# Performance work log

Hardware: AMD Instinct MI355X
Metric: run time of the kernel (lower is better)

Reference implementation:

```python
import jax, jax.numpy as jnp
import numpy as np

B, D = 4096, 512
BASE_TAU = 0.02
CLAMP_MAX = 1e36


def _l2norm(x, eps=1e-12):
    # torch F.normalize(p=2): x / max(||x||, eps)
    n = jnp.sqrt(jnp.sum(x * x, axis=-1, keepdims=True))
    return x / jnp.maximum(n, eps)


def setup_inputs() -> dict:
    key = jax.random.key(0)
    k1, k2, k3, k4, k5, k6 = jax.random.split(key, 6)
    return {
        "visual_feats": jax.random.normal(k1, (B, D), dtype=jnp.float32),
        "textual_feats": jax.random.normal(k2, (B, D), dtype=jnp.float32),
        "pid": jax.random.randint(k3, (B,), 0, 1024, dtype=jnp.int64 if jax.config.jax_enable_x64 else jnp.int32),
        "adaptive_margins": jax.random.uniform(k4, (B,), dtype=jnp.float32),
        "uncertainty_scores": jax.random.uniform(k5, (B,), dtype=jnp.float32),
        "sample_types": jax.random.randint(k6, (B,), 0, 3, dtype=jnp.int64 if jax.config.jax_enable_x64 else jnp.int32),
    }


def reference(visual_feats, textual_feats, pid, adaptive_margins, uncertainty_scores, sample_types):
    tau = BASE_TAU
    vn = _l2norm(visual_feats)
    tn = _l2norm(textual_feats)
    scores = tn @ vn.T  # [B, B]

    # Faithful to the original loop: every iteration i builds a [B,B] matrix
    # whose rows are all scores[i,:] and uses the FULL pid vector, then takes
    # row 0 of the per-sample loss. So the label/mask row is always pid[0]'s.
    labels0 = (pid == pid[0]).astype(scores.dtype)  # [B]
    mask0 = 1.0 - labels0                            # [B]
    n_neg0 = jnp.sum(mask0)

    margins = jax.lax.stop_gradient(adaptive_margins)  # .item() in torch -> no grad

    e = jnp.exp(scores / tau)  # [B, B]
    # i2t branch (row 0 of expanded matrix == scores[i,:], mask row = mask0)
    alpha = jax.lax.stop_gradient(e * labels0 / jnp.sum(e * labels0, axis=1, keepdims=True))  # [B,B]
    neg_sum = jnp.minimum(jnp.sum(e * mask0, axis=1), CLAMP_MAX)  # [B]
    loss_i2t = jnp.maximum(-jnp.sum(alpha * scores, axis=1) + tau * jnp.log(neg_sum) + margins, 0.0)

    # t2i branch: row 0 of expanded.T is scores[i,0] repeated B times;
    # alpha_t2i row 0 sums to 1 so -(alpha*s).sum == -scores[i,0].
    s0 = scores[:, 0]  # [B]
    t2i_sum = jnp.minimum(jnp.exp(s0 / tau) * n_neg0, CLAMP_MAX)
    loss_t2i = jnp.maximum(-s0 + tau * jnp.log(t2i_sum) + margins, 0.0)

    per_sample_losses = loss_i2t + loss_t2i  # [B]

    uncertain = sample_types == 2
    uncertainty_weights = jnp.where(
        uncertain,
        jnp.clip(1.0 - 0.5 * uncertainty_scores, 0.1, 1.0),
        jnp.ones_like(uncertainty_scores),
    )
    final_loss = jnp.sum(per_sample_losses * uncertainty_weights) / jnp.sum(uncertainty_weights)
    return final_loss, per_sample_losses, uncertainty_weights, scores
```

## Files before the change

### kernel.cpp

```cpp
#include <hip/hip_runtime.h>
#include <hip/hip_bf16.h>
#include <stdint.h>

#define NB 4096
#define ND 512
#define TAU_ 0.02f
#define INV_TAU_ 50.0f
#define CLAMP_MAXF 1e36f

typedef __attribute__((ext_vector_type(8))) short bf16x8;
typedef __attribute__((ext_vector_type(4))) float f32x4;

#define AS1(p) ((__attribute__((address_space(1))) void*)(uintptr_t)(p))
#define AS3(p) ((__attribute__((address_space(3))) void*)(uint32_t)(uintptr_t)(p))

static __device__ __forceinline__ unsigned short f2bf(float f) {
  __hip_bfloat16 h = __float2bfloat16(f);
  return *reinterpret_cast<unsigned short*>(&h);
}

__global__ __launch_bounds__(256) void k_norm(const float* __restrict__ vis,
                                              const float* __restrict__ txt,
                                              const int* __restrict__ pid,
                                              unsigned short* __restrict__ tn_b,
                                              unsigned short* __restrict__ vn_b,
                                              float* __restrict__ nneg) {
  if (blockIdx.x == 2048) {
    __shared__ float r4[4];
    int tid = threadIdx.x;
    int pid0 = pid[0];
    float c = 0.f;
    for (int j = tid; j < NB; j += 256) c += (pid[j] != pid0) ? 1.0f : 0.0f;
#pragma unroll
    for (int o = 32; o; o >>= 1) c += __shfl_xor(c, o, 64);
    if ((tid & 63) == 0) r4[tid >> 6] = c;
    __syncthreads();
    if (tid == 0) nneg[0] = r4[0] + r4[1] + r4[2] + r4[3];
    return;
  }
  int wv = threadIdx.x >> 6, ln = threadIdx.x & 63;
  int r = blockIdx.x * 4 + wv;
  const float* src;
  unsigned short* dst;
  if (r < NB) {
    src = txt + (size_t)r * ND;
    dst = tn_b + (size_t)r * ND;
  } else {
    src = vis + (size_t)(r - NB) * ND;
    dst = vn_b + (size_t)(r - NB) * ND;
  }
  float4 x0 = reinterpret_cast<const float4*>(src)[ln];
  float4 x1 = reinterpret_cast<const float4*>(src)[64 + ln];
  float ss = x0.x * x0.x + x0.y * x0.y + x0.z * x0.z + x0.w * x0.w +
             x1.x * x1.x + x1.y * x1.y + x1.z * x1.z + x1.w * x1.w;
#pragma unroll
  for (int o = 32; o; o >>= 1) ss += __shfl_xor(ss, o, 64);
  float inv = 1.0f / fmaxf(sqrtf(ss), 1e-12f);
  ushort4 p0, p1;
  p0.x = f2bf(x0.x * inv); p0.y = f2bf(x0.y * inv);
  p0.z = f2bf(x0.z * inv); p0.w = f2bf(x0.w * inv);
  p1.x = f2bf(x1.x * inv); p1.y = f2bf(x1.y * inv);
  p1.z = f2bf(x1.z * inv); p1.w = f2bf(x1.w * inv);
  reinterpret_cast<ushort4*>(dst)[ln] = p0;
  reinterpret_cast<ushort4*>(dst)[64 + ln] = p1;
}

__global__ __launch_bounds__(512, 2) void k_gemm(const unsigned short* __restrict__ A,
                                                 const unsigned short* __restrict__ Bm,
                                                 const int* __restrict__ pid,
                                                 float* __restrict__ C,
                                                 float* __restrict__ partials) {
  __shared__ unsigned short smem[2][2][256 * 64];
  int tid = threadIdx.x;
  int wv = tid >> 6, ln = tid & 63;
  int bm = blockIdx.x >> 4;
  int bn = blockIdx.x & 15;
  int wr = wv >> 2, wc = wv & 3;
  int frow = ln & 15, fkg = ln >> 4;
  f32x4 acc[8][4] = {};
  const unsigned short* Abase = A + (size_t)(bm * 256) * ND;
  const unsigned short* Bbase = Bm + (size_t)(bn * 256) * ND;

#define STAGE(buf, k0)                                                          \
  {                                                                             \
    _Pragma("unroll") for (int p = 0; p < 4; ++p) {                             \
      int s = p * 512 + tid;                                                    \
      int rr = s >> 3;                                                          \
      int slot = (s & 7) ^ (rr & 7);            \
      __builtin_amdgcn_global_load_lds(                                         \
          AS1(Abase + (size_t)rr * ND + (k0) + slot * 8),                       \
          AS3((char*)&smem[buf][0][0] + (p * 512 + wv * 64) * 16), 16, 0, 0);   \
      __builtin_amdgcn_global_load_lds(                                         \
          AS1(Bbase + (size_t)rr * ND + (k0) + slot * 8),                       \
          AS3((char*)&smem[buf][1][0] + (p * 512 + wv * 64) * 16), 16, 0, 0);   \
    }                                                                           \
  }

  STAGE(0, 0);
  __syncthreads();
  int buf = 0;
  for (int t = 0; t < 8; ++t) {
    if (t < 7) STAGE(buf ^ 1, (t + 1) * 64);
    const char* pA = (const char*)&smem[buf][0][0];
    const char* pB = (const char*)&smem[buf][1][0];
#pragma unroll
    for (int ksub = 0; ksub < 2; ++ksub) {
      bf16x8 af[8], bfr[4];
#pragma unroll
      for (int mi = 0; mi < 8; ++mi) {
        int row = wr * 128 + mi * 16 + frow;
        af[mi] = *reinterpret_cast<const bf16x8*>(
            pA + row * 128 + (((ksub * 4 + fkg) ^ (row & 7)) * 16));
      }
#pragma unroll
      for (int ni = 0; ni < 4; ++ni) {
        int row = wc * 64 + ni * 16 + frow;
        bfr[ni] = *reinterpret_cast<const bf16x8*>(
            pB + row * 128 + (((ksub * 4 + fkg) ^ (row & 7)) * 16));
      }
#pragma unroll
      for (int mi = 0; mi < 8; ++mi)
#pragma unroll
        for (int ni = 0; ni < 4; ++ni)
          acc[mi][ni] = __builtin_amdgcn_mfma_f32_16x16x32_bf16(af[mi], bfr[ni],
                                                                acc[mi][ni], 0, 0, 0);
    }
    __syncthreads();
    buf ^= 1;
  }

  int pid0 = pid[0];
  int eq[4];
#pragma unroll
  for (int ni = 0; ni < 4; ++ni)
    eq[ni] = (pid[bn * 256 + wc * 64 + ni * 16 + frow] == pid0) ? 1 : 0;

  float* pb = reinterpret_cast<float*>(&smem[0][0][0]);
  float* Cp = C + (size_t)(bm * 256 + wr * 128 + fkg * 4) * NB + bn * 256 +
              wc * 64 + frow;
#pragma unroll
  for (int mi = 0; mi < 8; ++mi) {
#pragma unroll
    for (int v = 0; v < 4; ++v) {
      float sp = 0.f, sn = 0.f, sa = 0.f;
      float* rp = Cp + (size_t)(mi * 16 + v) * NB;
#pragma unroll
      for (int ni = 0; ni < 4; ++ni) {
        float s = acc[mi][ni][v];
        rp[ni * 16] = s;
        float e = __expf(s * INV_TAU_);
        if (eq[ni]) {
          sp += e;
          sa += e * s;
        } else {
          sn += e;
        }
      }
#pragma unroll
      for (int o = 1; o < 16; o <<= 1) {
        sp += __shfl_xor(sp, o, 64);
        sn += __shfl_xor(sn, o, 64);
        sa += __shfl_xor(sa, o, 64);
      }
      if (frow == 0) {
        int row = wr * 128 + mi * 16 + fkg * 4 + v;
        pb[(wc * 256 + row) * 3 + 0] = sp;
        pb[(wc * 256 + row) * 3 + 1] = sn;
        pb[(wc * 256 + row) * 3 + 2] = sa;
      }
    }
  }
  __syncthreads();
  if (tid < 256) {
    float sp = 0.f, sn = 0.f, sa = 0.f;
#pragma unroll
    for (int w = 0; w < 4; ++w) {
      sp += pb[(w * 256 + tid) * 3 + 0];
      sn += pb[(w * 256 + tid) * 3 + 1];
      sa += pb[(w * 256 + tid) * 3 + 2];
    }
    float* pout = partials + ((size_t)(bm * 256 + tid) * 16 + bn) * 3;
    pout[0] = sp;
    pout[1] = sn;
    pout[2] = sa;
  }
}

__global__ __launch_bounds__(256) void k_row2(const float* __restrict__ partials,
                                              const float* __restrict__ scores,
                                              const float* __restrict__ margins,
                                              const float* __restrict__ unc,
                                              const int* __restrict__ stypes,
                                              const float* __restrict__ nneg,
                                              float* __restrict__ psl,
                                              float* __restrict__ uw) {
  int wv = threadIdx.x >> 6, ln = threadIdx.x & 63;
  int row = blockIdx.x * 4 + wv;
  const float* p = partials + (size_t)row * 16 * 3;
  float sp = 0.f, sn = 0.f, sa = 0.f;
  if (ln < 16) {
    sp = p[ln * 3 + 0];
    sn = p[ln * 3 + 1];
    sa = p[ln * 3 + 2];
  }
#pragma unroll
  for (int o = 1; o < 16; o <<= 1) {
    sp += __shfl_xor(sp, o, 64);
    sn += __shfl_xor(sn, o, 64);
    sa += __shfl_xor(sa, o, 64);
  }
  if (ln == 0) {
    float s0v = scores[(size_t)row * NB];
    float m = margins[row];
    float li2t = fmaxf(-(sa / sp) + TAU_ * logf(fminf(sn, CLAMP_MAXF)) + m, 0.f);
    float t2i = fminf(__expf(s0v * INV_TAU_) * nneg[0], CLAMP_MAXF);
    float lt2i = fmaxf(-s0v + TAU_ * logf(t2i) + m, 0.f);
    psl[row] = li2t + lt2i;
    float w = 1.f;
    if (stypes[row] == 2) w = fminf(fmaxf(1.f - 0.5f * unc[row], 0.1f), 1.f);
    uw[row] = w;
  }
}

__global__ __launch_bounds__(256) void k_final(const float* __restrict__ psl,
                                               const float* __restrict__ uw,
                                               float* __restrict__ out) {
  __shared__ float rn[4], rd[4];
  int tid = threadIdx.x;
  float num = 0.f, den = 0.f;
  for (int j = tid; j < NB; j += 256) {
    float w = uw[j];
    num += psl[j] * w;
    den += w;
  }
#pragma unroll
  for (int o = 32; o; o >>= 1) {
    num += __shfl_xor(num, o, 64);
    den += __shfl_xor(den, o, 64);
  }
  if ((tid & 63) == 0) {
    rn[tid >> 6] = num;
    rd[tid >> 6] = den;
  }
  __syncthreads();
  if (tid == 0) {
    num = rn[0] + rn[1] + rn[2] + rn[3];
    den = rd[0] + rd[1] + rd[2] + rd[3];
    out[0] = num / den;
  }
}

extern "C" void kernel_launch(void* const* d_in, const int* in_sizes, int n_in,
                              void* d_out, int out_size, void* d_ws, size_t ws_size,
                              hipStream_t stream) {
  const float* vis = (const float*)d_in[0];
  const float* txt = (const float*)d_in[1];
  const int* pid = (const int*)d_in[2];
  const float* margins = (const float*)d_in[3];
  const float* unc = (const float*)d_in[4];
  const int* stypes = (const int*)d_in[5];

  float* out = (float*)d_out;
  float* out_psl = out + 1;
  float* out_uw = out + 1 + NB;
  float* out_scores = out + 1 + 2 * NB;

  unsigned short* tn_b = (unsigned short*)d_ws;
  unsigned short* vn_b = tn_b + (size_t)NB * ND;
  float* nneg = (float*)(vn_b + (size_t)NB * ND);
  float* partials = nneg + 4;

  k_norm<<<2049, 256, 0, stream>>>(vis, txt, pid, tn_b, vn_b, nneg);
  k_gemm<<<256, 512, 0, stream>>>(tn_b, vn_b, pid, out_scores, partials);
  k_row2<<<NB / 4, 256, 0, stream>>>(partials, out_scores, margins, unc, stypes,
                                     nneg, out_psl, out_uw);
  k_final<<<1, 256, 0, stream>>>(out_psl, out_uw, out);
}
```

Measured before the change: 51.01 us.

## Deepen GEMM K-pipeline to 4-stage ring with BK=32, tile swizzle and setprio

Restructures the GEMM main loop from a double-buffered BK=64 scheme into a 4-buffer ring of BK=32 stages, keeping two loads in flight and synchronising with explicit vmcnt waits and a single barrier per step. It also changes the LDS swizzle to a rotation pattern suited to 64-byte rows, remaps block indices so neighbouring blocks share A/B tiles in cache, and raises wave priority around the MFMA burst. The aim is to hide global-to-LDS latency better and cut barrier overhead. The handwritten vmcnt counts are fragile and the per-step MFMA work is halved.

```diff
diff --git a/kernel.cpp b/kernel.cpp
--- a/kernel.cpp
+++ b/kernel.cpp
@@ -70,64 +70,67 @@
                                                  const int* __restrict__ pid,
                                                  float* __restrict__ C,
                                                  float* __restrict__ partials) {
-  __shared__ unsigned short smem[2][2][256 * 64];
+  __shared__ unsigned short smem[4][2][256 * 32];
   int tid = threadIdx.x;
   int wv = tid >> 6, ln = tid & 63;
-  int bm = blockIdx.x >> 4;
-  int bn = blockIdx.x & 15;
+  int tile = (blockIdx.x & 7) * 32 + (blockIdx.x >> 3);
+  int bm = tile >> 4;
+  int bn = tile & 15;
   int wr = wv >> 2, wc = wv & 3;
   int frow = ln & 15, fkg = ln >> 4;
   f32x4 acc[8][4] = {};
   const unsigned short* Abase = A + (size_t)(bm * 256) * ND;
   const unsigned short* Bbase = Bm + (size_t)(bn * 256) * ND;
 
-#define STAGE(buf, k0)                                                          \
+#define STAGE(bidx, k0)                                                         \
   {                                                                             \
-    _Pragma("unroll") for (int p = 0; p < 4; ++p) {                             \
+    _Pragma("unroll") for (int p = 0; p < 2; ++p) {                             \
       int s = p * 512 + tid;                                                    \
-      int rr = s >> 3;                                                          \
-      int slot = (s & 7) ^ (rr & 7);            \
+      int rr = s >> 2;                                                          \
+      int sg = ((s & 3) + (rr >> 1)) & 3;                                       \
       __builtin_amdgcn_global_load_lds(                                         \
-          AS1(Abase + (size_t)rr * ND + (k0) + slot * 8),                       \
-          AS3((char*)&smem[buf][0][0] + (p * 512 + wv * 64) * 16), 16, 0, 0);   \
+          AS1(Abase + (size_t)rr * ND + (k0) + sg * 8),                         \
+          AS3((char*)&smem[bidx][0][0] + (p * 512 + wv * 64) * 16), 16, 0, 0);  \
       __builtin_amdgcn_global_load_lds(                                         \
-          AS1(Bbase + (size_t)rr * ND + (k0) + slot * 8),                       \
-          AS3((char*)&smem[buf][1][0] + (p * 512 + wv * 64) * 16), 16, 0, 0);   \
+          AS1(Bbase + (size_t)rr * ND + (k0) + sg * 8),                         \
+          AS3((char*)&smem[bidx][1][0] + (p * 512 + wv * 64) * 16), 16, 0, 0);  \
     }                                                                           \
   }
 
+#define COMPUTE(bidx)                                                           \
+  {                                                                             \
+    const char* pA = (const char*)&smem[bidx][0][0];                            \
+    const char* pB = (const char*)&smem[bidx][1][0];                            \
+    bf16x8 af[8], bfr[4];                                                       \
+    _Pragma("unroll") for (int mi = 0; mi < 8; ++mi) {                          \
+      int row = wr * 128 + mi * 16 + frow;                                      \
+      af[mi] = *reinterpret_cast<const bf16x8*>(                                \
+          pA + row * 64 + (((fkg - (row >> 1)) & 3) * 16));                     \
+    }                                                                           \
+    _Pragma("unroll") for (int ni = 0; ni < 4; ++ni) {                          \
+      int row = wc * 64 + ni * 16 + frow;                                       \
+      bfr[ni] = *reinterpret_cast<const bf16x8*>(                               \
+          pB + row * 64 + (((fkg - (row >> 1)) & 3) * 16));                     \
+    }                                                                           \
+    __builtin_amdgcn_s_setprio(1);                                              \
+    _Pragma("unroll") for (int mi = 0; mi < 8; ++mi)                            \
+      _Pragma("unroll") for (int ni = 0; ni < 4; ++ni)                          \
+        acc[mi][ni] = __builtin_amdgcn_mfma_f32_16x16x32_bf16(af[mi], bfr[ni],  \
+                                                              acc[mi][ni], 0, 0, 0); \
+    __builtin_amdgcn_s_setprio(0);                                              \
+  }
+
   STAGE(0, 0);
-  __syncthreads();
-  int buf = 0;
-  for (int t = 0; t < 8; ++t) {
-    if (t < 7) STAGE(buf ^ 1, (t + 1) * 64);
-    const char* pA = (const char*)&smem[buf][0][0];
-    const char* pB = (const char*)&smem[buf][1][0];
-#pragma unroll
-    for (int ksub = 0; ksub < 2; ++ksub) {
-      bf16x8 af[8], bfr[4];
-#pragma unroll
-      for (int mi = 0; mi < 8; ++mi) {
-        int row = wr * 128 + mi * 16 + frow;
-        af[mi] = *reinterpret_cast<const bf16x8*>(
-            pA + row * 128 + (((ksub * 4 + fkg) ^ (row & 7)) * 16));
-      }
-#pragma unroll
-      for (int ni = 0; ni < 4; ++ni) {
-        int row = wc * 64 + ni * 16 + frow;
-        bfr[ni] = *reinterpret_cast<const bf16x8*>(
-            pB + row * 128 + (((ksub * 4 + fkg) ^ (row & 7)) * 16));
-      }
-#pragma unroll
-      for (int mi = 0; mi < 8; ++mi)
-#pragma unroll
-        for (int ni = 0; ni < 4; ++ni)
-          acc[mi][ni] = __builtin_amdgcn_mfma_f32_16x16x32_bf16(af[mi], bfr[ni],
-                                                                acc[mi][ni], 0, 0, 0);
-    }
-    __syncthreads();
-    buf ^= 1;
-  }
+  STAGE(1, 32);
+  for (int t = 0; t < 15; ++t) {
+    asm volatile("s_waitcnt vmcnt(4)" ::: "memory");
+    __builtin_amdgcn_s_barrier();
+    if (t < 14) STAGE((t + 2) & 3, (t + 2) * 32);
+    COMPUTE(t & 3);
+  }
+  asm volatile("s_waitcnt vmcnt(0)" ::: "memory");
+  __builtin_amdgcn_s_barrier();
+  COMPUTE(3);
 
   int pid0 = pid[0];
   int eq[4];
```

After: 52.14 us. 2.2% more time.

## Add dedicated producer wave with LDS flag handshake for GEMM K-loop loads

Applied to the files above, without the earlier changes.

Adds a ninth wavefront to the GEMM block that only issues global-to-LDS loads into the double buffer. It signals compute waves through workgroup-scope atomic flags instead of block-wide __syncthreads, so loads overlap MFMA work without a full-block barrier each K step. The change also swizzles block-to-tile mapping, writes per-wave partials straight to global memory (64 per row, reduced in k_row2) instead of through LDS, and exports column-0 scores to a small buffer. The costs are spin-wait polling, lower occupancy from the 576-thread block without the min-blocks hint, and more partial-sum traffic.

```diff
diff --git a/kernel.cpp b/kernel.cpp
--- a/kernel.cpp
+++ b/kernel.cpp
@@ -65,53 +65,70 @@
   reinterpret_cast<ushort4*>(dst)[64 + ln] = p1;
 }
 
-__global__ __launch_bounds__(512, 2) void k_gemm(const unsigned short* __restrict__ A,
-                                                 const unsigned short* __restrict__ Bm,
-                                                 const int* __restrict__ pid,
-                                                 float* __restrict__ C,
-                                                 float* __restrict__ partials) {
+__global__ __launch_bounds__(576) void k_gemm(const unsigned short* __restrict__ A,
+                                              const unsigned short* __restrict__ Bm,
+                                              const int* __restrict__ pid,
+                                              float* __restrict__ C,
+                                              float* __restrict__ partials,
+                                              float* __restrict__ s0g) {
   __shared__ unsigned short smem[2][2][256 * 64];
+  __shared__ unsigned int flg[4];
   int tid = threadIdx.x;
   int wv = tid >> 6, ln = tid & 63;
-  int bm = blockIdx.x >> 4;
-  int bn = blockIdx.x & 15;
+  int tile = (blockIdx.x & 7) * 32 + (blockIdx.x >> 3);
+  int bm = tile >> 4, bn = tile & 15;
+  const unsigned short* Abase = A + (size_t)(bm * 256) * ND;
+  const unsigned short* Bbase = Bm + (size_t)(bn * 256) * ND;
+  if (tid < 4) flg[tid] = 0;
+  __syncthreads();
+
+  if (wv == 8) {
+    int lanerow = ln >> 3;
+    int slot = (ln & 7) ^ (lanerow & 7);
+    const unsigned short* srcA = Abase + (size_t)lanerow * ND + slot * 8;
+    const unsigned short* srcB = Bbase + (size_t)lanerow * ND + slot * 8;
+    for (int j = 0; j < 8; ++j) {
+      if (j >= 2) {
+        unsigned need = (unsigned)((j >> 1) * 8);
+        while (__hip_atomic_load(&flg[2 + (j & 1)], __ATOMIC_ACQUIRE,
+                                 __HIP_MEMORY_SCOPE_WORKGROUP) < need)
+          __builtin_amdgcn_s_sleep(1);
+      }
+      int b = j & 1;
+      const unsigned short* sA = srcA + j * 64;
+      const unsigned short* sB = srcB + j * 64;
+      char* dA = (char*)&smem[b][0][0];
+      char* dB = (char*)&smem[b][1][0];
+#pragma unroll 8
+      for (int i = 0; i < 32; ++i)
+        __builtin_amdgcn_global_load_lds(AS1(sA + (size_t)i * 8 * ND),
+                                         AS3(dA + i * 1024), 16, 0, 0);
+#pragma unroll 8
+      for (int i = 0; i < 32; ++i)
+        __builtin_amdgcn_global_load_lds(AS1(sB + (size_t)i * 8 * ND),
+                                         AS3(dB + i * 1024), 16, 0, 0);
+      asm volatile("s_waitcnt vmcnt(0)" ::: "memory");
+      __builtin_amdgcn_sched_barrier(0);
+      __hip_atomic_store(&flg[b], (unsigned)(j + 1), __ATOMIC_RELEASE,
+                         __HIP_MEMORY_SCOPE_WORKGROUP);
+    }
+    return;
+  }
+
   int wr = wv >> 2, wc = wv & 3;
   int frow = ln & 15, fkg = ln >> 4;
   f32x4 acc[8][4] = {};
-  const unsigned short* Abase = A + (size_t)(bm * 256) * ND;
-  const unsigned short* Bbase = Bm + (size_t)(bn * 256) * ND;
-
-#define STAGE(buf, k0)                                                          \
-  {                                                                             \
-    _Pragma("unroll") for (int p = 0; p < 4; ++p) {                             \
-      int s = p * 512 + tid;                                                    \
-      int rr = s >> 3;                                                          \
-      int slot = (s & 7) ^ (rr & 7);            \
-      __builtin_amdgcn_global_load_lds(                                         \
-          AS1(Abase + (size_t)rr * ND + (k0) + slot * 8),                       \
-          AS3((char*)&smem[buf][0][0] + (p * 512 + wv * 64) * 16), 16, 0, 0);   \
-      __builtin_amdgcn_global_load_lds(                                         \
-          AS1(Bbase + (size_t)rr * ND + (k0) + slot * 8),                       \
-          AS3((char*)&smem[buf][1][0] + (p * 512 + wv * 64) * 16), 16, 0, 0);   \
-    }                                                                           \
-  }
-
-  STAGE(0, 0);
-  __syncthreads();
-  int buf = 0;
-  for (int t = 0; t < 8; ++t) {
-    if (t < 7) STAGE(buf ^ 1, (t + 1) * 64);
-    const char* pA = (const char*)&smem[buf][0][0];
-    const char* pB = (const char*)&smem[buf][1][0];
+
+  for (int j = 0; j < 8; ++j) {
+    while (__hip_atomic_load(&flg[j & 1], __ATOMIC_ACQUIRE,
+                             __HIP_MEMORY_SCOPE_WORKGROUP) < (unsigned)(j + 1))
+      __builtin_amdgcn_s_sleep(1);
+    __builtin_amdgcn_sched_barrier(0);
+    const char* pA = (const char*)&smem[j & 1][0][0];
+    const char* pB = (const char*)&smem[j & 1][1][0];
 #pragma unroll
     for (int ksub = 0; ksub < 2; ++ksub) {
-      bf16x8 af[8], bfr[4];
-#pragma unroll
-      for (int mi = 0; mi < 8; ++mi) {
-        int row = wr * 128 + mi * 16 + frow;
-        af[mi] = *reinterpret_cast<const bf16x8*>(
-            pA + row * 128 + (((ksub * 4 + fkg) ^ (row & 7)) * 16));
-      }
+      bf16x8 bfr[4];
 #pragma unroll
       for (int ni = 0; ni < 4; ++ni) {
         int row = wc * 64 + ni * 16 + frow;
@@ -119,14 +136,21 @@
             pB + row * 128 + (((ksub * 4 + fkg) ^ (row & 7)) * 16));
       }
 #pragma unroll
-      for (int mi = 0; mi < 8; ++mi)
+      for (int mi = 0; mi < 8; ++mi) {
+        int row = wr * 128 + mi * 16 + frow;
+        bf16x8 a_ = *reinterpret_cast<const bf16x8*>(
+            pA + row * 128 + (((ksub * 4 + fkg) ^ (row & 7)) * 16));
 #pragma unroll
         for (int ni = 0; ni < 4; ++ni)
-          acc[mi][ni] = __builtin_amdgcn_mfma_f32_16x16x32_bf16(af[mi], bfr[ni],
-                                                                acc[mi][ni], 0, 0, 0);
+          acc[mi][ni] = __builtin_amdgcn_mfma_f32_16x16x32_bf16(a_, bfr[ni],
+                                                               acc[mi][ni], 0, 0, 0);
+      }
     }
-    __syncthreads();
-    buf ^= 1;
+    asm volatile("s_waitcnt lgkmcnt(0)" ::: "memory");
+    __builtin_amdgcn_sched_barrier(0);
+    if (ln == 0)
+      __hip_atomic_fetch_add(&flg[2 + (j & 1)], 1u, __ATOMIC_RELEASE,
+                             __HIP_MEMORY_SCOPE_WORKGROUP);
   }
 
   int pid0 = pid[0];
@@ -134,8 +158,6 @@
 #pragma unroll
   for (int ni = 0; ni < 4; ++ni)
     eq[ni] = (pid[bn * 256 + wc * 64 + ni * 16 + frow] == pid0) ? 1 : 0;
-
-  float* pb = reinterpret_cast<float*>(&smem[0][0][0]);
   float* Cp = C + (size_t)(bm * 256 + wr * 128 + fkg * 4) * NB + bn * 256 +
               wc * 64 + frow;
 #pragma unroll
@@ -163,31 +185,19 @@
         sa += __shfl_xor(sa, o, 64);
       }
       if (frow == 0) {
-        int row = wr * 128 + mi * 16 + fkg * 4 + v;
-        pb[(wc * 256 + row) * 3 + 0] = sp;
-        pb[(wc * 256 + row) * 3 + 1] = sn;
-        pb[(wc * 256 + row) * 3 + 2] = sa;
+        int row = bm * 256 + wr * 128 + mi * 16 + fkg * 4 + v;
+        float* po = partials + ((size_t)row * 64 + bn * 4 + wc) * 3;
+        po[0] = sp;
+        po[1] = sn;
+        po[2] = sa;
+        if (bn == 0 && wc == 0) s0g[row] = acc[mi][0][v];
       }
     }
   }
-  __syncthreads();
-  if (tid < 256) {
-    float sp = 0.f, sn = 0.f, sa = 0.f;
-#pragma unroll
-    for (int w = 0; w < 4; ++w) {
-      sp += pb[(w * 256 + tid) * 3 + 0];
-      sn += pb[(w * 256 + tid) * 3 + 1];
-      sa += pb[(w * 256 + tid) * 3 + 2];
-    }
-    float* pout = partials + ((size_t)(bm * 256 + tid) * 16 + bn) * 3;
-    pout[0] = sp;
-    pout[1] = sn;
-    pout[2] = sa;
-  }
 }
 
 __global__ __launch_bounds__(256) void k_row2(const float* __restrict__ partials,
-                                              const float* __restrict__ scores,
+                                              const float* __restrict__ s0g,
                                               const float* __restrict__ margins,
                                               const float* __restrict__ unc,
                                               const int* __restrict__ stypes,
@@ -196,21 +206,16 @@
                                               float* __restrict__ uw) {
   int wv = threadIdx.x >> 6, ln = threadIdx.x & 63;
   int row = blockIdx.x * 4 + wv;
-  const float* p = partials + (size_t)row * 16 * 3;
-  float sp = 0.f, sn = 0.f, sa = 0.f;
-  if (ln < 16) {
-    sp = p[ln * 3 + 0];
-    sn = p[ln * 3 + 1];
-    sa = p[ln * 3 + 2];
-  }
-#pragma unroll
-  for (int o = 1; o < 16; o <<= 1) {
+  const float* p = partials + (size_t)row * 64 * 3 + ln * 3;
+  float sp = p[0], sn = p[1], sa = p[2];
+#pragma unroll
+  for (int o = 1; o < 64; o <<= 1) {
     sp += __shfl_xor(sp, o, 64);
     sn += __shfl_xor(sn, o, 64);
     sa += __shfl_xor(sa, o, 64);
   }
   if (ln == 0) {
-    float s0v = scores[(size_t)row * NB];
+    float s0v = s0g[row];
     float m = margins[row];
     float li2t = fmaxf(-(sa / sp) + TAU_ * logf(fminf(sn, CLAMP_MAXF)) + m, 0.f);
     float t2i = fminf(__expf(s0v * INV_TAU_) * nneg[0], CLAMP_MAXF);
@@ -268,11 +273,12 @@
   unsigned short* tn_b = (unsigned short*)d_ws;
   unsigned short* vn_b = tn_b + (size_t)NB * ND;
   float* nneg = (float*)(vn_b + (size_t)NB * ND);
-  float* partials = nneg + 4;
+  float* s0g = nneg + 4;
+  float* partials = s0g + NB;
 
   k_norm<<<2049, 256, 0, stream>>>(vis, txt, pid, tn_b, vn_b, nneg);
-  k_gemm<<<256, 512, 0, stream>>>(tn_b, vn_b, pid, out_scores, partials);
-  k_row2<<<NB / 4, 256, 0, stream>>>(partials, out_scores, margins, unc, stypes,
+  k_gemm<<<256, 576, 0, stream>>>(tn_b, vn_b, pid, out_scores, partials, s0g);
+  k_row2<<<NB / 4, 256, 0, stream>>>(partials, s0g, margins, unc, stypes,
                                      nneg, out_psl, out_uw);
   k_final<<<1, 256, 0, stream>>>(out_psl, out_uw, out);
 }
```

Measured after the change: 66.85 us. +31.0%, slower.

## Remap GEMM tiles across XCDs, stream scores non-temporally, drop LDS epilogue reduction

Applied to the files above, without the earlier changes.

Block indices are remapped so that consecutive tiles sharing A/B panels land on the same XCD, aiming for better L2 reuse. The score matrix is now written with nontemporal stores so it does not pollute the cache. The in-block LDS reduction and its barrier are removed: each wave writes its own partial sums straight to global memory, and the row kernel reduces 64 partials per row. Column-0 scores go to a small side buffer so the row kernel no longer does strided reads from the large output. In exchange, the partials buffer is four times larger.

```diff
diff --git a/kernel.cpp b/kernel.cpp
--- a/kernel.cpp
+++ b/kernel.cpp
@@ -69,12 +69,14 @@
                                                  const unsigned short* __restrict__ Bm,
                                                  const int* __restrict__ pid,
                                                  float* __restrict__ C,
-                                                 float* __restrict__ partials) {
+                                                 float* __restrict__ partials,
+                                                 float* __restrict__ s0g) {
   __shared__ unsigned short smem[2][2][256 * 64];
   int tid = threadIdx.x;
   int wv = tid >> 6, ln = tid & 63;
-  int bm = blockIdx.x >> 4;
-  int bn = blockIdx.x & 15;
+  int tile = (blockIdx.x & 7) * 32 + (blockIdx.x >> 3);
+  int bm = tile >> 4;
+  int bn = tile & 15;
   int wr = wv >> 2, wc = wv & 3;
   int frow = ln & 15, fkg = ln >> 4;
   f32x4 acc[8][4] = {};
@@ -134,8 +136,6 @@
 #pragma unroll
   for (int ni = 0; ni < 4; ++ni)
     eq[ni] = (pid[bn * 256 + wc * 64 + ni * 16 + frow] == pid0) ? 1 : 0;
-
-  float* pb = reinterpret_cast<float*>(&smem[0][0][0]);
   float* Cp = C + (size_t)(bm * 256 + wr * 128 + fkg * 4) * NB + bn * 256 +
               wc * 64 + frow;
 #pragma unroll
@@ -147,7 +147,7 @@
 #pragma unroll
       for (int ni = 0; ni < 4; ++ni) {
         float s = acc[mi][ni][v];
-        rp[ni * 16] = s;
+        __builtin_nontemporal_store(s, rp + ni * 16);
         float e = __expf(s * INV_TAU_);
         if (eq[ni]) {
           sp += e;
@@ -163,31 +163,19 @@
         sa += __shfl_xor(sa, o, 64);
       }
       if (frow == 0) {
-        int row = wr * 128 + mi * 16 + fkg * 4 + v;
-        pb[(wc * 256 + row) * 3 + 0] = sp;
-        pb[(wc * 256 + row) * 3 + 1] = sn;
-        pb[(wc * 256 + row) * 3 + 2] = sa;
+        int row = bm * 256 + wr * 128 + mi * 16 + fkg * 4 + v;
+        float* po = partials + ((size_t)row * 64 + bn * 4 + wc) * 3;
+        po[0] = sp;
+        po[1] = sn;
+        po[2] = sa;
+        if (bn == 0 && wc == 0) s0g[row] = acc[mi][0][v];
       }
     }
   }
-  __syncthreads();
-  if (tid < 256) {
-    float sp = 0.f, sn = 0.f, sa = 0.f;
-#pragma unroll
-    for (int w = 0; w < 4; ++w) {
-      sp += pb[(w * 256 + tid) * 3 + 0];
-      sn += pb[(w * 256 + tid) * 3 + 1];
-      sa += pb[(w * 256 + tid) * 3 + 2];
-    }
-    float* pout = partials + ((size_t)(bm * 256 + tid) * 16 + bn) * 3;
-    pout[0] = sp;
-    pout[1] = sn;
-    pout[2] = sa;
-  }
 }
 
 __global__ __launch_bounds__(256) void k_row2(const float* __restrict__ partials,
-                                              const float* __restrict__ scores,
+                                              const float* __restrict__ s0g,
                                               const float* __restrict__ margins,
                                               const float* __restrict__ unc,
                                               const int* __restrict__ stypes,
@@ -196,21 +184,16 @@
                                               float* __restrict__ uw) {
   int wv = threadIdx.x >> 6, ln = threadIdx.x & 63;
   int row = blockIdx.x * 4 + wv;
-  const float* p = partials + (size_t)row * 16 * 3;
-  float sp = 0.f, sn = 0.f, sa = 0.f;
-  if (ln < 16) {
-    sp = p[ln * 3 + 0];
-    sn = p[ln * 3 + 1];
-    sa = p[ln * 3 + 2];
-  }
-#pragma unroll
-  for (int o = 1; o < 16; o <<= 1) {
+  const float* p = partials + (size_t)row * 64 * 3 + ln * 3;
+  float sp = p[0], sn = p[1], sa = p[2];
+#pragma unroll
+  for (int o = 1; o < 64; o <<= 1) {
     sp += __shfl_xor(sp, o, 64);
     sn += __shfl_xor(sn, o, 64);
     sa += __shfl_xor(sa, o, 64);
   }
   if (ln == 0) {
-    float s0v = scores[(size_t)row * NB];
+    float s0v = s0g[row];
     float m = margins[row];
     float li2t = fmaxf(-(sa / sp) + TAU_ * logf(fminf(sn, CLAMP_MAXF)) + m, 0.f);
     float t2i = fminf(__expf(s0v * INV_TAU_) * nneg[0], CLAMP_MAXF);
@@ -268,11 +251,12 @@
   unsigned short* tn_b = (unsigned short*)d_ws;
   unsigned short* vn_b = tn_b + (size_t)NB * ND;
   float* nneg = (float*)(vn_b + (size_t)NB * ND);
-  float* partials = nneg + 4;
+  float* s0g = nneg + 4;
+  float* partials = s0g + NB;
 
   k_norm<<<2049, 256, 0, stream>>>(vis, txt, pid, tn_b, vn_b, nneg);
-  k_gemm<<<256, 512, 0, stream>>>(tn_b, vn_b, pid, out_scores, partials);
-  k_row2<<<NB / 4, 256, 0, stream>>>(partials, out_scores, margins, unc, stypes,
+  k_gemm<<<256, 512, 0, stream>>>(tn_b, vn_b, pid, out_scores, partials, s0g);
+  k_row2<<<NB / 4, 256, 0, stream>>>(partials, s0g, margins, unc, stypes,
                                      nneg, out_psl, out_uw);
   k_final<<<1, 256, 0, stream>>>(out_psl, out_uw, out);
 }
```

New measurement: 69.51 us. +36.3%, slower.
